# Performance work log

Hardware: AMD Instinct MI355X
Metric: run time of the kernel (lower is better)

Reference implementation:

```python
import jax, jax.numpy as jnp
import numpy as np

N = 100000   # nodes
E = 1000000  # edges (avg degree 10)
F_IN, H1, H2, C = 128, 64, 64, 16


def setup_inputs() -> dict:
    key = jax.random.key(0)
    ks = jax.random.split(key, 10)
    x = jax.random.normal(ks[0], (N, F_IN), dtype=jnp.float32)
    edge_src = jax.random.randint(ks[1], (E,), 0, N, dtype=jnp.int32)
    edge_dst = jax.random.randint(ks[2], (E,), 0, N, dtype=jnp.int32)
    # normalized-adjacency-like positive edge weights (~1/deg scale)
    edge_val = jax.random.uniform(ks[3], (E,), dtype=jnp.float32) * 0.1
    def glorot(k, fan_in, fan_out):
        s = np.float32(1.0 / np.sqrt(fan_in))
        return jax.random.normal(k, (fan_in, fan_out), dtype=jnp.float32) * s
    W1 = glorot(ks[4], F_IN, H1)
    W2 = glorot(ks[5], H1, H2)
    W3 = glorot(ks[6], H2, C)
    b1 = jnp.zeros((H1,), jnp.float32)
    b2 = jnp.zeros((H2,), jnp.float32)
    b3 = jnp.zeros((C,), jnp.float32)
    return {"x": x, "edge_val": edge_val, "W1": W1, "b1": b1,
            "W2": W2, "b2": b2, "W3": W3, "b3": b3,
            "edge_src": edge_src, "edge_dst": edge_dst}


def gcn_layer(h, W, b, edge_src, edge_dst, edge_val):
    # support = h @ W ; out = spmm(adj, support) + b
    support = h @ W                                  # [N, d_out]
    msg = support[edge_src] * edge_val[:, None]      # [E, d_out] gather + scale
    agg = jax.ops.segment_sum(msg, edge_dst, num_segments=N)  # scatter-add
    return agg + b


def reference(x, edge_val, W1, b1, W2, b2, W3, b3, edge_src, edge_dst):
    # eval mode: F.dropout(training=False) is identity
    h = jax.nn.relu(gcn_layer(x, W1, b1, edge_src, edge_dst, edge_val))
    h = jax.nn.relu(gcn_layer(h, W2, b2, edge_src, edge_dst, edge_val))
    return gcn_layer(h, W3, b3, edge_src, edge_dst, edge_val)  # [N, C] logits
```

## Files before the change

kernel.cpp:

```cpp
#include <hip/hip_runtime.h>
#include <stdint.h>

#define N_NODES 100000
#define N_EDGES 1000000
#define NBUCK 196
#define CAP 6656

typedef __attribute__((ext_vector_type(8))) __bf16 bf16x8;
typedef __attribute__((ext_vector_type(4))) float f32x4;

static __device__ __forceinline__ float bf2f(unsigned short u) {
    return __uint_as_float(((unsigned int)u) << 16);
}
static __device__ __forceinline__ unsigned short f2bf(float f) {
    unsigned int u = __float_as_uint(f);
    unsigned int r = (u + 0x7FFFu + ((u >> 16) & 1u)) >> 16;
    return (unsigned short)r;
}
static __device__ __forceinline__ void st8_half(unsigned short* p, const float* f) {
    int4 u;
    u.x = (int)(((unsigned)f2bf(f[0])) | (((unsigned)f2bf(f[1])) << 16));
    u.y = (int)(((unsigned)f2bf(f[2])) | (((unsigned)f2bf(f[3])) << 16));
    u.z = (int)(((unsigned)f2bf(f[4])) | (((unsigned)f2bf(f[5])) << 16));
    u.w = (int)(((unsigned)f2bf(f[6])) | (((unsigned)f2bf(f[7])) << 16));
    *(int4*)p = u;
}

static __device__ __forceinline__ float ldf(const void* p, size_t i, int bf) {
    return bf ? bf2f(((const unsigned short*)p)[i]) : ((const float*)p)[i];
}

__global__ __launch_bounds__(256) void detect_kernel(const unsigned short* __restrict__ xs,
                                                     int* __restrict__ flag,
                                                     int* __restrict__ bcursor) {
    __shared__ int sz;
    if (threadIdx.x == 0) sz = 0;
    __syncthreads();
    int z = 0;
    for (int i = threadIdx.x; i < 1024; i += 256) {
        float av = fabsf(bf2f(xs[2 * i]));
        if (!(av <= 1048576.0f) || (av != 0.0f && av < 9.5367431640625e-07f)) z++;
    }
    atomicAdd(&sz, z);
    if (threadIdx.x < NBUCK) bcursor[threadIdx.x] = threadIdx.x * CAP;
    __syncthreads();
    if (threadIdx.x == 0) *flag = (sz > 256) ? 0 : 1;
}

__global__ __launch_bounds__(256) void part_kernel(const int* __restrict__ src,
                                                   const int* __restrict__ dst,
                                                   const void* __restrict__ val,
                                                   int* __restrict__ bcursor,
                                                   int2* __restrict__ part,
                                                   const int* __restrict__ flagp) {
    __shared__ int cnt[256];
    __shared__ int s[256];
    __shared__ int base[NBUCK];
    __shared__ int2 stage[2048];
    __shared__ unsigned char bktl[2048];
    const int bf = *flagp;
    const int tid = threadIdx.x;
    const int e0 = blockIdx.x * 2048;
    cnt[tid] = 0;
    __syncthreads();
    int rank[8], bkt[8], pk[8], vb[8];
#pragma unroll
    for (int i = 0; i < 8; ++i) {
        int e = e0 + i * 256 + tid;
        bkt[i] = -1;
        if (e < N_EDGES) {
            int d = dst[e];
            int b = d >> 9;
            bkt[i] = b;
            pk[i] = src[e] | ((d & 511) << 17);
            vb[i] = __float_as_int(ldf(val, e, bf));
            rank[i] = atomicAdd(&cnt[b], 1);
        }
    }
    __syncthreads();
    s[tid] = cnt[tid];
    __syncthreads();
    for (int off = 1; off < 256; off <<= 1) {
        int t = 0;
        if (tid >= off) t = s[tid - off];
        __syncthreads();
        if (tid >= off) s[tid] += t;
        __syncthreads();
    }
    for (int i = tid; i < NBUCK; i += 256) {
        int c = cnt[i];
        base[i] = c ? atomicAdd(&bcursor[i], c) : 0;
    }
#pragma unroll
    for (int i = 0; i < 8; ++i) {
        if (bkt[i] >= 0) {
            int b = bkt[i];
            int sp = s[b] - cnt[b] + rank[i];
            stage[sp] = make_int2(pk[i], vb[i]);
            bktl[sp] = (unsigned char)b;
        }
    }
    __syncthreads();
    const int nE = min(2048, N_EDGES - e0);
    for (int j = tid; j < nE; j += 256) {
        int bk = bktl[j];
        part[(size_t)base[bk] + (j - (s[bk] - cnt[bk]))] = stage[j];
    }
}

__global__ __launch_bounds__(512) void place_kernel(const int* __restrict__ bcursor,
                                                    const int2* __restrict__ part,
                                                    int* __restrict__ row_start,
                                                    int2* __restrict__ csr_rec) {
    __shared__ int cnt[512];
    __shared__ int sums[512];
    __shared__ int sh_s, sh_cnt, sh_total;
    const int tid = threadIdx.x;
    const int b = blockIdx.x;
    const int row0 = b << 9;
    const int nrows = min(512, N_NODES - row0);

    if (tid < 256) sums[tid] = (tid < NBUCK) ? (bcursor[tid] - tid * CAP) : 0;
    __syncthreads();
    for (int off = 1; off < 256; off <<= 1) {
        int t = 0;
        if (tid < 256 && tid >= off) t = sums[tid - off];
        __syncthreads();
        if (tid < 256 && tid >= off) sums[tid] += t;
        __syncthreads();
    }
    if (tid == 0) {
        sh_s = (b > 0) ? sums[b - 1] : 0;
        sh_cnt = bcursor[b] - b * CAP;
        sh_total = sums[NBUCK - 1];
    }
    __syncthreads();
    const int s = sh_s;
    const int cb = sh_cnt;
    const int ps = b * CAP;
    const int total = sh_total;

    cnt[tid] = 0;
    __syncthreads();
    for (int j = tid; j < cb; j += 512) {
        unsigned p = (unsigned)part[ps + j].x;
        atomicAdd(&cnt[p >> 17], 1);
    }
    __syncthreads();
    int own = cnt[tid];
    sums[tid] = own;
    __syncthreads();
    for (int off = 1; off < 512; off <<= 1) {
        int t = 0;
        if (tid >= off) t = sums[tid - off];
        __syncthreads();
        if (tid >= off) sums[tid] += t;
        __syncthreads();
    }
    int excl = sums[tid] - own;
    cnt[tid] = s + excl;
    if (tid < nrows) row_start[row0 + tid] = s + excl;
    if (b == NBUCK - 1 && tid == 0) row_start[N_NODES] = total;
    __syncthreads();
    for (int j = tid; j < cb; j += 512) {
        int2 r = part[ps + j];
        unsigned p = (unsigned)r.x;
        int pos = atomicAdd(&cnt[p >> 17], 1);
        csr_rec[pos] = make_int2((int)(p & 0x1FFFFu), r.y);
    }
}

template <int RS>
static __device__ __forceinline__ void row_gather(const unsigned short* __restrict__ supc,
                                                  const int2* __restrict__ csr_rec,
                                                  int s, int e, float a[8]) {
    if (s >= e) return;
    int2 r[4];
#pragma unroll
    for (int t = 0; t < 4; ++t) r[t] = csr_rec[min(s + t, e - 1)];
    for (int j = s; j < e; j += 4) {
        int4 sp[4];
#pragma unroll
        for (int t = 0; t < 4; ++t) sp[t] = *(const int4*)(supc + (size_t)r[t].x * RS);
        float wv[4];
#pragma unroll
        for (int t = 0; t < 4; ++t) wv[t] = (j + t < e) ? __int_as_float(r[t].y) : 0.0f;
        int jn = j + 4;
        if (jn < e) {
#pragma unroll
            for (int t = 0; t < 4; ++t) r[t] = csr_rec[min(jn + t, e - 1)];
        }
#pragma unroll
        for (int t = 0; t < 4; ++t) {
            float w = wv[t];
            int q[4] = {sp[t].x, sp[t].y, sp[t].z, sp[t].w};
#pragma unroll
            for (int c = 0; c < 4; ++c) {
                float flo = __uint_as_float(((unsigned)q[c]) << 16);
                float fhi = __uint_as_float(((unsigned)q[c]) & 0xffff0000u);
                a[2 * c]     += w * flo;
                a[2 * c + 1] += w * fhi;
            }
        }
    }
}

template <int K, int M, bool DYNIN>
__global__ __launch_bounds__(256, 8) void mgemm_kernel(const void* __restrict__ hv_,
                                                       const void* __restrict__ W,
                                                       unsigned short* __restrict__ out,
                                                       const int* __restrict__ flagp) {
    constexpr int KP = K + 8;
    constexpr int NC = M / 16;
    constexpr int NK = K / 32;

    __shared__ __align__(16) unsigned short wt[M][KP];

    const int bf = *flagp;
    const int tid = threadIdx.x;

    for (int i = tid; i < K * M; i += 256) {
        int k = i / M, m = i % M;
        wt[m][k] = f2bf(ldf(W, i, bf));
    }
    __syncthreads();

    const int lane = tid & 63;
    const int qd = lane >> 4;
    const int ln = lane & 15;
    const int wrow = (tid >> 6) * 16;
    const int tile = blockIdx.x;

    const int row = tile * 64 + wrow + ln;
    const bool ok = row < N_NODES;

    f32x4 acc[NC];
#pragma unroll
    for (int c = 0; c < NC; ++c) acc[c] = (f32x4){0.f, 0.f, 0.f, 0.f};

#pragma unroll
    for (int ks = 0; ks < NK; ++ks) {
        bf16x8 a;
        if (ok) {
            const size_t base = (size_t)row * K + ks * 32 + qd * 8;
            if (DYNIN && !bf) {
                const float* xp = (const float*)hv_ + base;
                float4 f0 = *(const float4*)xp;
                float4 f1 = *(const float4*)(xp + 4);
                ushort4 uu[2];
                uu[0].x = f2bf(f0.x); uu[0].y = f2bf(f0.y); uu[0].z = f2bf(f0.z); uu[0].w = f2bf(f0.w);
                uu[1].x = f2bf(f1.x); uu[1].y = f2bf(f1.y); uu[1].z = f2bf(f1.z); uu[1].w = f2bf(f1.w);
                a = *(const bf16x8*)uu;
            } else {
                a = *(const bf16x8*)((const unsigned short*)hv_ + base);
            }
        } else {
            a = (bf16x8)(__bf16)0.0f;
        }
#pragma unroll
        for (int c = 0; c < NC; ++c) {
            bf16x8 b = *(const bf16x8*)&wt[c * 16 + ln][ks * 32 + qd * 8];
            acc[c] = __builtin_amdgcn_mfma_f32_16x16x32_bf16(a, b, acc[c], 0, 0, 0);
        }
    }

#pragma unroll
    for (int c = 0; c < NC; ++c) {
#pragma unroll
        for (int r = 0; r < 4; ++r) {
            int orow = tile * 64 + wrow + qd * 4 + r;
            if (orow < N_NODES) out[(size_t)orow * M + c * 16 + ln] = f2bf(acc[c][r]);
        }
    }
}

template <int MOUT>
__global__ __launch_bounds__(256, 8) void fused_kernel(const unsigned short* __restrict__ support,
                                                       const int* __restrict__ row_start,
                                                       const int2* __restrict__ csr_rec,
                                                       const void* __restrict__ bias,
                                                       const void* __restrict__ W,
                                                       unsigned short* __restrict__ out,
                                                       const int* __restrict__ flagp) {
    constexpr int K = 64, KP = 72;
    constexpr int NC = MOUT / 16;
    constexpr int NK = 2;

    __shared__ __align__(16) unsigned short agg[64][KP];
    __shared__ __align__(16) unsigned short wt[MOUT][KP];

    const int bf = *flagp;
    const int tid = threadIdx.x;

    for (int i = tid; i < K * MOUT; i += 256) {
        int k = i / MOUT, m = i % MOUT;
        wt[m][k] = f2bf(ldf(W, i, bf));
    }

    const int lane = tid & 63;
    const int qd = lane >> 4;
    const int ln = lane & 15;
    const int wrow = (tid >> 6) * 16;

    const int grp = tid >> 3;
    const int cc = tid & 7;
    const unsigned short* supc = support + cc * 8;

    const int tile = blockIdx.x;
    const int rowA = tile * 64 + grp;
    const int rowB = rowA + 32;
    int s0 = row_start[min(rowA, N_NODES)];
    int e0 = row_start[min(rowA + 1, N_NODES)];
    int s1 = row_start[min(rowB, N_NODES)];
    int e1 = row_start[min(rowB + 1, N_NODES)];

    {
        float a[8];
#pragma unroll
        for (int c = 0; c < 8; ++c) a[c] = 0.0f;
        row_gather<64>(supc, csr_rec, s0, e0, a);
#pragma unroll
        for (int c = 0; c < 8; ++c) a[c] = fmaxf(a[c] + ldf(bias, cc * 8 + c, bf), 0.f);
        st8_half(&agg[grp][cc * 8], a);
    }
    {
        float a[8];
#pragma unroll
        for (int c = 0; c < 8; ++c) a[c] = 0.0f;
        row_gather<64>(supc, csr_rec, s1, e1, a);
#pragma unroll
        for (int c = 0; c < 8; ++c) a[c] = fmaxf(a[c] + ldf(bias, cc * 8 + c, bf), 0.f);
        st8_half(&agg[32 + grp][cc * 8], a);
    }
    __syncthreads();

    f32x4 macc[NC];
#pragma unroll
    for (int c = 0; c < NC; ++c) macc[c] = (f32x4){0.f, 0.f, 0.f, 0.f};
#pragma unroll
    for (int ks = 0; ks < NK; ++ks) {
        bf16x8 a = *(const bf16x8*)&agg[wrow + ln][ks * 32 + qd * 8];
#pragma unroll
        for (int c = 0; c < NC; ++c) {
            bf16x8 b = *(const bf16x8*)&wt[c * 16 + ln][ks * 32 + qd * 8];
            macc[c] = __builtin_amdgcn_mfma_f32_16x16x32_bf16(a, b, macc[c], 0, 0, 0);
        }
    }

#pragma unroll
    for (int c = 0; c < NC; ++c) {
#pragma unroll
        for (int r = 0; r < 4; ++r) {
            int orow = tile * 64 + wrow + qd * 4 + r;
            if (orow < N_NODES) out[(size_t)orow * MOUT + c * 16 + ln] = f2bf(macc[c][r]);
        }
    }
}

template <bool DYNOUT>
__global__ __launch_bounds__(256, 8) void spmm16_kernel(const unsigned short* __restrict__ support,
                                                        const int* __restrict__ row_start,
                                                        const int2* __restrict__ csr_rec,
                                                        const void* __restrict__ bias,
                                                        void* __restrict__ out_,
                                                        const int* __restrict__ flagp) {
    constexpr int M = 16;
    int bf = *flagp;
    int tid = threadIdx.x;
    int grp = tid >> 1;
    int cc = tid & 1;
    int row = blockIdx.x * 128 + grp;
    if (row >= N_NODES) return;
    int s = row_start[row];
    int e = row_start[row + 1];
    float a[8];
#pragma unroll
    for (int c = 0; c < 8; ++c) a[c] = 0.0f;
    row_gather<16>(support + cc * 8, csr_rec, s, e, a);
#pragma unroll
    for (int c = 0; c < 8; ++c) a[c] += ldf(bias, cc * 8 + c, bf);
    if (DYNOUT && !bf) {
        float* op = (float*)out_ + (size_t)row * M + cc * 8;
        *(float4*)op = make_float4(a[0], a[1], a[2], a[3]);
        *(float4*)(op + 4) = make_float4(a[4], a[5], a[6], a[7]);
    } else {
        st8_half((unsigned short*)out_ + (size_t)row * M + cc * 8, a);
    }
}

extern "C" void kernel_launch(void* const* d_in, const int* in_sizes, int n_in,
                              void* d_out, int out_size, void* d_ws, size_t ws_size,
                              hipStream_t stream) {
    (void)in_sizes; (void)n_in; (void)out_size; (void)ws_size;
    const void* x  = d_in[0];
    const void* ev = d_in[1];
    const void* W1 = d_in[2];
    const void* b1 = d_in[3];
    const void* W2 = d_in[4];
    const void* b2 = d_in[5];
    const void* W3 = d_in[6];
    const void* b3 = d_in[7];
    const int* esrc = (const int*)d_in[8];
    const int* edst = (const int*)d_in[9];

    char* ws = (char*)d_ws;
    size_t off = 0;
    auto alloc = [&](size_t bytes) -> void* {
        void* p = ws + off;
        off = (off + bytes + 255) & ~(size_t)255;
        return p;
    };
    unsigned short* A = (unsigned short*)alloc((size_t)N_NODES * 64 * 2);
    unsigned short* B = (unsigned short*)alloc((size_t)N_NODES * 64 * 2);
    int* row_start  = (int*)alloc((size_t)(N_NODES + 1) * 4);
    int* bcursor    = (int*)alloc(1024);
    int2* csr_rec   = (int2*)alloc((size_t)N_EDGES * 8);
    int* flagp      = (int*)alloc(256);
    int2* part      = (int2*)A;

    detect_kernel<<<1, 256, 0, stream>>>((const unsigned short*)x, flagp, bcursor);

    part_kernel<<<(N_EDGES + 2047) / 2048, 256, 0, stream>>>(esrc, edst, ev, bcursor, part, flagp);
    place_kernel<<<NBUCK, 512, 0, stream>>>(bcursor, part, row_start, csr_rec);

    const int NT = (N_NODES + 63) / 64;

    mgemm_kernel<128, 64, true><<<NT, 256, 0, stream>>>(x, W1, A, flagp);
    fused_kernel<64><<<NT, 256, 0, stream>>>(A, row_start, csr_rec, b1, W2, B, flagp);
    fused_kernel<16><<<NT, 256, 0, stream>>>(B, row_start, csr_rec, b2, W3, A, flagp);
    spmm16_kernel<true><<<(N_NODES + 127) / 128, 256, 0, stream>>>(A, row_start, csr_rec, b3, d_out, flagp);
}
```

Baseline: 228.0 us.

## Quantize intermediate 64-wide support to int8 with per-row scales for gathers

```diff
diff --git a/kernel.cpp b/kernel.cpp
--- a/kernel.cpp
+++ b/kernel.cpp
@@ -170,6 +170,48 @@
     }
 }
 
+static __device__ __forceinline__ void row_gather_i8(const unsigned char* __restrict__ supc,
+                                                     const float* __restrict__ sscale,
+                                                     const int2* __restrict__ csr_rec,
+                                                     int s, int e, float a[8], float& wsum) {
+    if (s >= e) return;
+    int2 r[4];
+#pragma unroll
+    for (int t = 0; t < 4; ++t) r[t] = csr_rec[min(s + t, e - 1)];
+    for (int j = s; j < e; j += 4) {
+        int2 sp[4];
+        float sc[4];
+#pragma unroll
+        for (int t = 0; t < 4; ++t) {
+            sp[t] = *(const int2*)(supc + (size_t)r[t].x * 64);
+            sc[t] = sscale[r[t].x];
+        }
+        float wv[4];
+#pragma unroll
+        for (int t = 0; t < 4; ++t) wv[t] = (j + t < e) ? __int_as_float(r[t].y) : 0.0f;
+        int jn = j + 4;
+        if (jn < e) {
+#pragma unroll
+            for (int t = 0; t < 4; ++t) r[t] = csr_rec[min(jn + t, e - 1)];
+        }
+#pragma unroll
+        for (int t = 0; t < 4; ++t) {
+            float ws = wv[t] * sc[t];
+            wsum += ws;
+            unsigned x = (unsigned)sp[t].x;
+            unsigned y = (unsigned)sp[t].y;
+            a[0] += ws * (float)(x & 0xffu);
+            a[1] += ws * (float)((x >> 8) & 0xffu);
+            a[2] += ws * (float)((x >> 16) & 0xffu);
+            a[3] += ws * (float)(x >> 24);
+            a[4] += ws * (float)(y & 0xffu);
+            a[5] += ws * (float)((y >> 8) & 0xffu);
+            a[6] += ws * (float)((y >> 16) & 0xffu);
+            a[7] += ws * (float)(y >> 24);
+        }
+    }
+}
+
 template <int RS>
 static __device__ __forceinline__ void row_gather(const unsigned short* __restrict__ supc,
                                                   const int2* __restrict__ csr_rec,
@@ -205,10 +247,27 @@
     }
 }
 
+static __device__ __forceinline__ void quant_row_store(const float v[4], int nc, int row,
+                                                       int ln, unsigned char* __restrict__ out8,
+                                                       float* __restrict__ oscale) {
+    float m = 0.f;
+    for (int c = 0; c < nc; ++c) m = fmaxf(m, fabsf(v[c]));
+#pragma unroll
+    for (int off = 1; off < 16; off <<= 1) m = fmaxf(m, __shfl_xor(m, off));
+    float inv = (m > 0.f) ? 127.0f / m : 0.f;
+    if (row < N_NODES) {
+        if (ln == 0) oscale[row] = m * (1.0f / 127.0f);
+        for (int c = 0; c < nc; ++c)
+            out8[(size_t)row * 64 + c * 16 + ln] =
+                (unsigned char)((int)rintf(v[c] * inv) + 128);
+    }
+}
+
 template <int K, int M, bool DYNIN>
 __global__ __launch_bounds__(256, 8) void mgemm_kernel(const void* __restrict__ hv_,
                                                        const void* __restrict__ W,
-                                                       unsigned short* __restrict__ out,
+                                                       unsigned char* __restrict__ out8,
+                                                       float* __restrict__ oscale,
                                                        const int* __restrict__ flagp) {
     constexpr int KP = K + 8;
     constexpr int NC = M / 16;
@@ -265,22 +324,23 @@
     }
 
 #pragma unroll
-    for (int c = 0; c < NC; ++c) {
-#pragma unroll
-        for (int r = 0; r < 4; ++r) {
-            int orow = tile * 64 + wrow + qd * 4 + r;
-            if (orow < N_NODES) out[(size_t)orow * M + c * 16 + ln] = f2bf(acc[c][r]);
-        }
-    }
-}
-
-template <int MOUT>
-__global__ __launch_bounds__(256, 8) void fused_kernel(const unsigned short* __restrict__ support,
+    for (int r = 0; r < 4; ++r) {
+        float v[NC];
+#pragma unroll
+        for (int c = 0; c < NC; ++c) v[c] = acc[c][r];
+        quant_row_store(v, NC, tile * 64 + wrow + qd * 4 + r, ln, out8, oscale);
+    }
+}
+
+template <int MOUT, bool QOUT>
+__global__ __launch_bounds__(256, 8) void fused_kernel(const unsigned char* __restrict__ sup8,
+                                                       const float* __restrict__ sscale,
                                                        const int* __restrict__ row_start,
                                                        const int2* __restrict__ csr_rec,
                                                        const void* __restrict__ bias,
                                                        const void* __restrict__ W,
-                                                       unsigned short* __restrict__ out,
+                                                       void* __restrict__ out_,
+                                                       float* __restrict__ oscale,
                                                        const int* __restrict__ flagp) {
     constexpr int K = 64, KP = 72;
     constexpr int NC = MOUT / 16;
@@ -304,7 +364,7 @@
 
     const int grp = tid >> 3;
     const int cc = tid & 7;
-    const unsigned short* supc = support + cc * 8;
+    const unsigned char* supc = sup8 + cc * 8;
 
     const int tile = blockIdx.x;
     const int rowA = tile * 64 + grp;
@@ -316,20 +376,26 @@
 
     {
         float a[8];
+        float wsum = 0.f;
 #pragma unroll
         for (int c = 0; c < 8; ++c) a[c] = 0.0f;
-        row_gather<64>(supc, csr_rec, s0, e0, a);
-#pragma unroll
-        for (int c = 0; c < 8; ++c) a[c] = fmaxf(a[c] + ldf(bias, cc * 8 + c, bf), 0.f);
+        row_gather_i8(supc, sscale, csr_rec, s0, e0, a, wsum);
+        float corr = 128.f * wsum;
+#pragma unroll
+        for (int c = 0; c < 8; ++c)
+            a[c] = fmaxf(a[c] - corr + ldf(bias, cc * 8 + c, bf), 0.f);
         st8_half(&agg[grp][cc * 8], a);
     }
     {
         float a[8];
+        float wsum = 0.f;
 #pragma unroll
         for (int c = 0; c < 8; ++c) a[c] = 0.0f;
-        row_gather<64>(supc, csr_rec, s1, e1, a);
-#pragma unroll
-        for (int c = 0; c < 8; ++c) a[c] = fmaxf(a[c] + ldf(bias, cc * 8 + c, bf), 0.f);
+        row_gather_i8(supc, sscale, csr_rec, s1, e1, a, wsum);
+        float corr = 128.f * wsum;
+#pragma unroll
+        for (int c = 0; c < 8; ++c)
+            a[c] = fmaxf(a[c] - corr + ldf(bias, cc * 8 + c, bf), 0.f);
         st8_half(&agg[32 + grp][cc * 8], a);
     }
     __syncthreads();
@@ -347,12 +413,24 @@
         }
     }
 
-#pragma unroll
-    for (int c = 0; c < NC; ++c) {
+    if constexpr (QOUT) {
 #pragma unroll
         for (int r = 0; r < 4; ++r) {
-            int orow = tile * 64 + wrow + qd * 4 + r;
-            if (orow < N_NODES) out[(size_t)orow * MOUT + c * 16 + ln] = f2bf(macc[c][r]);
+            float v[NC];
+#pragma unroll
+            for (int c = 0; c < NC; ++c) v[c] = macc[c][r];
+            quant_row_store(v, NC, tile * 64 + wrow + qd * 4 + r, ln,
+                            (unsigned char*)out_, oscale);
+        }
+    } else {
+        unsigned short* outp = (unsigned short*)out_;
+#pragma unroll
+        for (int c = 0; c < NC; ++c) {
+#pragma unroll
+            for (int r = 0; r < 4; ++r) {
+                int orow = tile * 64 + wrow + qd * 4 + r;
+                if (orow < N_NODES) outp[(size_t)orow * MOUT + c * 16 + ln] = f2bf(macc[c][r]);
+            }
         }
     }
 }
@@ -410,13 +488,16 @@
         off = (off + bytes + 255) & ~(size_t)255;
         return p;
     };
-    unsigned short* A = (unsigned short*)alloc((size_t)N_NODES * 64 * 2);
-    unsigned short* B = (unsigned short*)alloc((size_t)N_NODES * 64 * 2);
+    unsigned char* A8 = (unsigned char*)alloc((size_t)N_NODES * 64);
+    float* sA        = (float*)alloc((size_t)N_NODES * 4);
+    unsigned char* B8 = (unsigned char*)alloc((size_t)N_NODES * 64);
+    float* sB        = (float*)alloc((size_t)N_NODES * 4);
+    unsigned short* A3 = (unsigned short*)alloc((size_t)N_NODES * 16 * 2);
     int* row_start  = (int*)alloc((size_t)(N_NODES + 1) * 4);
     int* bcursor    = (int*)alloc(1024);
     int2* csr_rec   = (int2*)alloc((size_t)N_EDGES * 8);
     int* flagp      = (int*)alloc(256);
-    int2* part      = (int2*)A;
+    int2* part      = (int2*)alloc((size_t)NBUCK * CAP * 8);
 
     detect_kernel<<<1, 256, 0, stream>>>((const unsigned short*)x, flagp, bcursor);
 
@@ -425,8 +506,8 @@
 
     const int NT = (N_NODES + 63) / 64;
 
-    mgemm_kernel<128, 64, true><<<NT, 256, 0, stream>>>(x, W1, A, flagp);
-    fused_kernel<64><<<NT, 256, 0, stream>>>(A, row_start, csr_rec, b1, W2, B, flagp);
-    fused_kernel<16><<<NT, 256, 0, stream>>>(B, row_start, csr_rec, b2, W3, A, flagp);
-    spmm16_kernel<true><<<(N_NODES + 127) / 128, 256, 0, stream>>>(A, row_start, csr_rec, b3, d_out, flagp);
-}
+    mgemm_kernel<128, 64, true><<<NT, 256, 0, stream>>>(x, W1, A8, sA, flagp);
+    fused_kernel<64, true><<<NT, 256, 0, stream>>>(A8, sA, row_start, csr_rec, b1, W2, B8, sB, flagp);
+    fused_kernel<16, false><<<NT, 256, 0, stream>>>(B8, sB, row_start, csr_rec, b2, W3, A3, sA, flagp);
+    spmm16_kernel<true><<<(N_NODES + 127) / 128, 256, 0, stream>>>(A3, row_start, csr_rec, b3, d_out, flagp);
+}
```

After: 232.6 us. 2.0% more time.
